# Performance work log

Measured on AMD Instinct MI355X. Metric: run time of the kernel, lower is better.

## Reference

```python
import jax, jax.numpy as jnp
import numpy as np

WS = 8        # window_size
NH = 12       # num_heads


def setup_inputs() -> dict:
    key = jax.random.key(0)
    ks = jax.random.split(key, 9)
    B, C, H, W = 4, 384, 128, 128
    s = 1.0 / np.sqrt(C)
    x = jax.random.normal(ks[0], (B, C, H, W), dtype=jnp.float32)
    Wq = jax.random.normal(ks[1], (C, C), dtype=jnp.float32) * s
    bq = jax.random.normal(ks[2], (C,), dtype=jnp.float32) * 0.01
    Wk = jax.random.normal(ks[3], (C, C), dtype=jnp.float32) * s
    bk = jax.random.normal(ks[4], (C,), dtype=jnp.float32) * 0.01
    Wv = jax.random.normal(ks[5], (C, C), dtype=jnp.float32) * s
    bv = jax.random.normal(ks[6], (C,), dtype=jnp.float32) * 0.01
    Wp = jax.random.normal(ks[7], (C, C), dtype=jnp.float32) * s
    bp = jax.random.normal(ks[8], (C,), dtype=jnp.float32) * 0.01
    return {"x": x, "Wq": Wq, "bq": bq, "Wk": Wk, "bk": bk,
            "Wv": Wv, "bv": bv, "Wp": Wp, "bp": bp}


def reference(x, Wq, bq, Wk, bk, Wv, bv, Wp, bp):
    B, C, H, W = x.shape
    ws2 = WS * WS
    dk = C // NH
    scale = dk ** -0.5

    # window_partition: flat row-major reshape (same semantics as torch's
    # reshape on a contiguous [B,C,H,W] tensor), then permute+view.
    p = x.reshape(B, H // WS, WS, W // WS, WS, C)
    p = jnp.transpose(p, (0, 5, 1, 3, 2, 4))          # [B, C, H/ws, W/ws, ws, ws]
    p = p.reshape(B, C, -1, ws2)                       # [B, C, nW, ws*ws]

    def conv1x1(w, b):  # 1x1 Conv2d on [B,C,nW,ws2]
        return jnp.einsum('bcnw,oc->bonw', p, w) + b[None, :, None, None]

    def heads(t):  # permute(0,2,3,1).contiguous().reshape -> [B, NH, nW, ws2, dk]
        t = jnp.transpose(t, (0, 2, 3, 1))             # [B, nW, ws2, C]
        return t.reshape(B, NH, -1, ws2, dk)           # row-major reinterpretation

    q = heads(conv1x1(Wq, bq))
    k = heads(conv1x1(Wk, bk))
    v = heads(conv1x1(Wv, bv))

    scores = jnp.einsum('bhnqd,bhnkd->bhnqk', q, k) * scale
    attn = jax.nn.softmax(scores, axis=-1)
    o = jnp.einsum('bhnqk,bhnkd->bhnqd', attn, v)      # [B, NH, nW, ws2, dk]
    o = o.reshape(B, -1, ws2, C)                       # [B, nW, ws2, C]

    # window_unpartition
    u = o.reshape(B, -1, WS, WS, C)
    u = jnp.transpose(u, (0, 4, 1, 2, 3))              # [B, C, nW, ws, ws]
    u = u.reshape(B, C, H, W)

    y = jnp.einsum('bchw,oc->bohw', u, Wp) + bp[None, :, None, None]
    return y
```

## Files before the change

kernel.cpp:

```cpp
#include <hip/hip_runtime.h>
#include <hip/hip_bf16.h>
#include <stdint.h>


typedef __bf16 bf16_t;
typedef __bf16 bf16x8 __attribute__((ext_vector_type(8)));
typedef float f32x4 __attribute__((ext_vector_type(4)));

__device__ __forceinline__ void gload_lds16(const void* g, void* l) {
  __builtin_amdgcn_global_load_lds((__attribute__((address_space(1))) void*)(g),
                                   (__attribute__((address_space(3))) void*)(l),
                                   16, 0, 0);
}

__global__ __launch_bounds__(256) void convw_kernel(
    const float* __restrict__ wq, const float* __restrict__ wk,
    const float* __restrict__ wv, const float* __restrict__ wp,
    bf16_t* __restrict__ oq, bf16_t* __restrict__ ok,
    bf16_t* __restrict__ ov, bf16_t* __restrict__ op_) {
  int i = blockIdx.x * 256 + threadIdx.x;
  oq[i] = (bf16_t)wq[i];
  ok[i] = (bf16_t)wk[i];
  ov[i] = (bf16_t)wv[i];
  op_[i] = (bf16_t)wp[i];
}

__device__ __forceinline__ void stageB(const bf16_t* __restrict__ B,
                                       bf16_t* Bs, int k0, int tid) {
  const int lane = tid & 63, wvv = tid >> 6;
  const int s = (lane & 3) ^ ((lane >> 3) & 3);
#pragma unroll
  for (int j = 0; j < 2; ++j) {
    int q = wvv * 128 + j * 64 + lane;
    int row = q >> 2;
    gload_lds16(B + (size_t)row * 384 + k0 + s * 8,
                (char*)Bs + (wvv * 128 + j * 64) * 16);
  }
}

struct ARegs { float4 v0, v1, v2, v3; };

__device__ __forceinline__ ARegs issueA(const float* __restrict__ xr0,
                                        const float* __restrict__ xr1, int k0) {
  ARegs a;
  a.v0 = *(const float4*)(xr0 + k0);
  a.v1 = *(const float4*)(xr0 + k0 + 4);
  a.v2 = *(const float4*)(xr1 + k0);
  a.v3 = *(const float4*)(xr1 + k0 + 4);
  return a;
}

__device__ __forceinline__ void writeA(const ARegs& a, bf16_t* Ab,
                                       int r0loc, int ssw) {
  bf16x8 p0, p1;
  p0[0] = (bf16_t)a.v0.x; p0[1] = (bf16_t)a.v0.y;
  p0[2] = (bf16_t)a.v0.z; p0[3] = (bf16_t)a.v0.w;
  p0[4] = (bf16_t)a.v1.x; p0[5] = (bf16_t)a.v1.y;
  p0[6] = (bf16_t)a.v1.z; p0[7] = (bf16_t)a.v1.w;
  p1[0] = (bf16_t)a.v2.x; p1[1] = (bf16_t)a.v2.y;
  p1[2] = (bf16_t)a.v2.z; p1[3] = (bf16_t)a.v2.w;
  p1[4] = (bf16_t)a.v3.x; p1[5] = (bf16_t)a.v3.y;
  p1[6] = (bf16_t)a.v3.z; p1[7] = (bf16_t)a.v3.w;
  *(bf16x8*)(Ab + r0loc * 32 + ssw * 8) = p0;
  *(bf16x8*)(Ab + (r0loc + 16) * 32 + ssw * 8) = p1;
}

__global__ __launch_bounds__(256) void qkv_gemm(
    const float* __restrict__ x, const bf16_t* __restrict__ Wcat,
    const float* __restrict__ bq, const float* __restrict__ bk,
    const float* __restrict__ bv,
    bf16_t* __restrict__ Qs, bf16_t* __restrict__ Ks, bf16_t* __restrict__ Vs) {
  __shared__ __align__(16) bf16_t L[16384];
  const int tid = threadIdx.x;
  const int F = blockIdx.x;
  const int xcd = F & 7;
  const int t = F >> 3;
  const int j = t % 9;
  const int gq = t / 9;
  const int m0 = (gq * 8 + xcd) * 128;
  const int which = j / 3;
  const int cb = (j % 3) * 128;
  const float* bias = which == 0 ? bq : (which == 1 ? bk : bv);
  bf16_t* Out = which == 0 ? Qs : (which == 1 ? Ks : Vs);
  const bf16_t* Wrows = Wcat + (size_t)j * 128 * 384;

  const int lane = tid & 63, wvv = tid >> 6;
  const int l15 = lane & 15, hi = lane >> 4;
  const int wr = wvv >> 1, wc = wvv & 1;
  const int slot = hi ^ ((l15 >> 1) & 3);
  const int r0loc = wvv * 32 + (lane >> 2);
  const int ssw = (lane & 3) ^ ((lane >> 3) & 3);

  const int b = m0 >> 14;
  const int pp0 = m0 & 16383;
  auto prow = [&](int pp) {
    int n1 = pp >> 10, n3 = (pp >> 6) & 15, w2 = (pp >> 3) & 7, w4 = pp & 7;
    return (size_t)((b << 14) | (n1 << 10) | (w2 << 7) | (n3 << 3) | w4) * 384;
  };
  const float* xr0 = x + prow(pp0 + r0loc) + (lane & 3) * 8;
  const float* xr1 = x + prow(pp0 + r0loc + 16) + (lane & 3) * 8;

  ARegs st0 = issueA(xr0, xr1, 0);
  stageB(Wrows, L + 4096, 0, tid);
  ARegs st1 = issueA(xr0, xr1, 32);
  stageB(Wrows, L + 8192 + 4096, 32, tid);

  f32x4 acc[4][4] = {};
#pragma unroll
  for (int kt = 0; kt < 12; ++kt) {
    bf16_t* Ab = L + (kt & 1) * 8192;
    bf16_t* Bb = Ab + 4096;
    if (kt == 11) asm volatile("s_waitcnt vmcnt(0)" ::: "memory");
    else          asm volatile("s_waitcnt vmcnt(6)" ::: "memory");
    __builtin_amdgcn_sched_barrier(0);
    writeA((kt & 1) ? st1 : st0, Ab, r0loc, ssw);
    asm volatile("s_waitcnt lgkmcnt(0)" ::: "memory");
    __builtin_amdgcn_sched_barrier(0);
    __builtin_amdgcn_s_barrier();
    bf16x8 a[4], bfr[4];
#pragma unroll
    for (int i = 0; i < 4; ++i) {
      a[i] = *(const bf16x8*)(Ab + (wr * 64 + i * 16 + l15) * 32 + slot * 8);
      bfr[i] = *(const bf16x8*)(Bb + (wc * 64 + i * 16 + l15) * 32 + slot * 8);
    }
#pragma unroll
    for (int mi = 0; mi < 4; ++mi)
#pragma unroll
      for (int ni = 0; ni < 4; ++ni)
        acc[mi][ni] = __builtin_amdgcn_mfma_f32_16x16x32_bf16(a[mi], bfr[ni],
                                                              acc[mi][ni], 0, 0, 0);
    asm volatile("s_waitcnt lgkmcnt(0)" ::: "memory");
    __builtin_amdgcn_sched_barrier(0);
    __builtin_amdgcn_s_barrier();
    if (kt + 2 < 12) {
      if (kt & 1) st1 = issueA(xr0, xr1, (kt + 2) * 32);
      else        st0 = issueA(xr0, xr1, (kt + 2) * 32);
      stageB(Wrows, Bb, (kt + 2) * 32, tid);
    }
  }

#pragma unroll
  for (int ni = 0; ni < 4; ++ni) {
    int ch = wc * 64 + ni * 16 + l15;
    float bv_ = bias[cb + ch];
#pragma unroll
    for (int mi = 0; mi < 4; ++mi)
#pragma unroll
      for (int r = 0; r < 4; ++r) {
        int row = wr * 64 + mi * 16 + hi * 4 + r;
        L[row * 128 + ch] = (bf16_t)(acc[mi][ni][r] + bv_);
      }
  }
  __syncthreads();
#pragma unroll
  for (int p = 0; p < 8; ++p) {
    int row = p * 16 + (tid >> 4);
    int ch = (tid & 15) * 8;
    bf16x8 val = *(const bf16x8*)(L + row * 128 + ch);
    *(bf16x8*)(Out + (size_t)(m0 + row) * 384 + cb + ch) = val;
  }
}

__device__ __forceinline__ void stage_tile(const bf16_t* __restrict__ A,
                                           const bf16_t* __restrict__ B,
                                           bf16_t* As, bf16_t* Bs, int k0, int tid) {
  const int lane = tid & 63, wvv = tid >> 6;
  const int s = (lane & 3) ^ ((lane >> 3) & 3);
#pragma unroll
  for (int j = 0; j < 2; ++j) {
    int q = wvv * 128 + j * 64 + lane;
    int row = q >> 2;
    gload_lds16(A + (size_t)row * 384 + k0 + s * 8,
                (char*)As + (wvv * 128 + j * 64) * 16);
    gload_lds16(B + (size_t)row * 384 + k0 + s * 8,
                (char*)Bs + (wvv * 128 + j * 64) * 16);
  }
}

__device__ __forceinline__ void gemm_mainloop(const bf16_t* __restrict__ Arows,
                                              const bf16_t* __restrict__ Brows,
                                              bf16_t* As, bf16_t* Bs,
                                              int tid, f32x4 acc[4][4]) {
  const int lane = tid & 63;
  const int l15 = lane & 15, hi = lane >> 4;
  const int wr = (tid >> 6) >> 1, wc = (tid >> 6) & 1;
  const int slot = hi ^ ((l15 >> 1) & 3);
  stage_tile(Arows, Brows, As, Bs, 0, tid);
  stage_tile(Arows, Brows, As + 4096, Bs + 4096, 32, tid);
#pragma unroll
  for (int kt = 0; kt < 12; ++kt) {
    bf16_t* Ab = As + (kt & 1) * 4096;
    bf16_t* Bb = Bs + (kt & 1) * 4096;
    if (kt == 11) asm volatile("s_waitcnt vmcnt(0)" ::: "memory");
    else          asm volatile("s_waitcnt vmcnt(4)" ::: "memory");
    __builtin_amdgcn_s_barrier();
    bf16x8 a[4], bfr[4];
#pragma unroll
    for (int i = 0; i < 4; ++i) {
      a[i] = *(const bf16x8*)(Ab + (wr * 64 + i * 16 + l15) * 32 + slot * 8);
      bfr[i] = *(const bf16x8*)(Bb + (wc * 64 + i * 16 + l15) * 32 + slot * 8);
    }
#pragma unroll
    for (int mi = 0; mi < 4; ++mi)
#pragma unroll
      for (int ni = 0; ni < 4; ++ni)
        acc[mi][ni] = __builtin_amdgcn_mfma_f32_16x16x32_bf16(a[mi], bfr[ni],
                                                              acc[mi][ni], 0, 0, 0);
    asm volatile("s_waitcnt lgkmcnt(0)" ::: "memory");
    __builtin_amdgcn_sched_barrier(0);
    __builtin_amdgcn_s_barrier();
    if (kt + 2 < 12)
      stage_tile(Arows, Brows, Ab, Bb, (kt + 2) * 32, tid);
  }
}

__global__ __launch_bounds__(64) void attn_kernel(const bf16_t* __restrict__ Q,
                                                  const bf16_t* __restrict__ K,
                                                  const bf16_t* __restrict__ V,
                                                  bf16_t* __restrict__ O) {
  const size_t base = (size_t)blockIdx.x * 2048;
  const bf16_t* q = Q + base;
  const bf16_t* k = K + base;
  const bf16_t* v = V + base;
  bf16_t* o = O + base;
  const int lane = threadIdx.x;
  const int l15 = lane & 15, hi = lane >> 4;

  __shared__ __align__(16) bf16_t Vt[32][72];
  __shared__ __align__(16) bf16_t Ps[64][72];

#pragma unroll
  for (int j = 0; j < 4; ++j) {
    bf16x8 vv = *(const bf16x8*)(v + lane * 32 + j * 8);
#pragma unroll
    for (int e = 0; e < 8; ++e) Vt[j * 8 + e][lane] = vv[e];
  }

  bf16x8 aQ[4], bK[4];
#pragma unroll
  for (int i = 0; i < 4; ++i) {
    aQ[i] = *(const bf16x8*)(q + (i * 16 + l15) * 32 + hi * 8);
    bK[i] = *(const bf16x8*)(k + (i * 16 + l15) * 32 + hi * 8);
  }
  f32x4 sc[4][4] = {};
#pragma unroll
  for (int mi = 0; mi < 4; ++mi)
#pragma unroll
    for (int ni = 0; ni < 4; ++ni)
      sc[mi][ni] = __builtin_amdgcn_mfma_f32_16x16x32_bf16(aQ[mi], bK[ni],
                                                           sc[mi][ni], 0, 0, 0);

  const float SCALE = 0.17677669529663687f;
  float rs[4][4];
#pragma unroll
  for (int mi = 0; mi < 4; ++mi) {
#pragma unroll
    for (int r = 0; r < 4; ++r) {
      float s0 = sc[mi][0][r] * SCALE, s1 = sc[mi][1][r] * SCALE;
      float s2 = sc[mi][2][r] * SCALE, s3 = sc[mi][3][r] * SCALE;
      float mx = fmaxf(fmaxf(s0, s1), fmaxf(s2, s3));
      mx = fmaxf(mx, __shfl_xor(mx, 1));
      mx = fmaxf(mx, __shfl_xor(mx, 2));
      mx = fmaxf(mx, __shfl_xor(mx, 4));
      mx = fmaxf(mx, __shfl_xor(mx, 8));
      float p0 = __expf(s0 - mx), p1 = __expf(s1 - mx);
      float p2 = __expf(s2 - mx), p3 = __expf(s3 - mx);
      int row = mi * 16 + hi * 4 + r;
      Ps[row][0 + l15] = (bf16_t)p0;
      Ps[row][16 + l15] = (bf16_t)p1;
      Ps[row][32 + l15] = (bf16_t)p2;
      Ps[row][48 + l15] = (bf16_t)p3;
      float sum = p0 + p1 + p2 + p3;
      sum += __shfl_xor(sum, 1);
      sum += __shfl_xor(sum, 2);
      sum += __shfl_xor(sum, 4);
      sum += __shfl_xor(sum, 8);
      rs[mi][r] = sum;
    }
  }
  __syncthreads();

  f32x4 oacc[4][2] = {};
#pragma unroll
  for (int mi = 0; mi < 4; ++mi)
#pragma unroll
    for (int ks = 0; ks < 2; ++ks) {
      bf16x8 aP = *(const bf16x8*)(&Ps[mi * 16 + l15][ks * 32 + hi * 8]);
#pragma unroll
      for (int n2 = 0; n2 < 2; ++n2) {
        bf16x8 bV = *(const bf16x8*)(&Vt[n2 * 16 + l15][ks * 32 + hi * 8]);
        oacc[mi][n2] = __builtin_amdgcn_mfma_f32_16x16x32_bf16(aP, bV,
                                                               oacc[mi][n2], 0, 0, 0);
      }
    }
#pragma unroll
  for (int mi = 0; mi < 4; ++mi)
#pragma unroll
    for (int n2 = 0; n2 < 2; ++n2)
#pragma unroll
      for (int r = 0; r < 4; ++r) {
        int row = mi * 16 + hi * 4 + r;
        o[row * 32 + n2 * 16 + l15] = (bf16_t)(oacc[mi][n2][r] / rs[mi][r]);
      }
}

__global__ __launch_bounds__(256) void proj_gemm(const bf16_t* __restrict__ Wpb,
                                                 const bf16_t* __restrict__ O,
                                                 const float* __restrict__ bp,
                                                 float* __restrict__ y) {
  __shared__ __align__(16) bf16_t As[2 * 128 * 32];
  __shared__ __align__(16) bf16_t Bs[2 * 128 * 32];
  const int tid = threadIdx.x;
  const int F = blockIdx.x;
  const int xcd = F & 7;
  const int t = F >> 3;
  const int j = t % 3;
  const int gq = t / 3;
  const int g = gq * 8 + xcd;
  const int n0 = (g & 127) * 128;
  const int b = g >> 7;
  const int m0 = j * 128;
  f32x4 acc[4][4] = {};
  gemm_mainloop(Wpb + (size_t)m0 * 384, O + ((size_t)b * 16384 + n0) * 384,
                As, Bs, tid, acc);
  const int lane = tid & 63, wvv = tid >> 6;
  const int l15 = lane & 15, hi = lane >> 4;
  const int wr = wvv >> 1, wc = wvv & 1;
  float* yb = y + (size_t)b * 6291456;
#pragma unroll
  for (int mi = 0; mi < 4; ++mi)
#pragma unroll
    for (int r = 0; r < 4; ++r) {
      int och = m0 + wr * 64 + mi * 16 + hi * 4 + r;
      float bpv = bp[och];
#pragma unroll
      for (int ni = 0; ni < 4; ++ni) {
        int pix = n0 + wc * 64 + ni * 16 + l15;
        yb[(size_t)och * 16384 + pix] = acc[mi][ni][r] + bpv;
      }
    }
}

extern "C" void kernel_launch(void* const* d_in, const int* in_sizes, int n_in,
                              void* d_out, int out_size, void* d_ws, size_t ws_size,
                              hipStream_t stream) {
  const float* x  = (const float*)d_in[0];
  const float* Wq = (const float*)d_in[1];
  const float* bq = (const float*)d_in[2];
  const float* Wk = (const float*)d_in[3];
  const float* bk = (const float*)d_in[4];
  const float* Wv = (const float*)d_in[5];
  const float* bv = (const float*)d_in[6];
  const float* Wp = (const float*)d_in[7];
  const float* bp = (const float*)d_in[8];
  float* y = (float*)d_out;

  char* ws = (char*)d_ws;
  const size_t SZ = 50331648;
  bf16_t* Ob  = (bf16_t*)(ws);
  bf16_t* Vs  = (bf16_t*)(ws + SZ);
  bf16_t* Wcat = (bf16_t*)(ws + 2 * SZ);
  bf16_t* Wkb = Wcat + 147456;
  bf16_t* Wvb = Wkb + 147456;
  bf16_t* Wpb = Wvb + 147456;
  bf16_t* Qs  = (bf16_t*)d_out;
  bf16_t* Ks  = (bf16_t*)((char*)d_out + SZ);

  convw_kernel<<<576, 256, 0, stream>>>(Wq, Wk, Wv, Wp, Wcat, Wkb, Wvb, Wpb);
  qkv_gemm<<<4608, 256, 0, stream>>>(x, Wcat, bq, bk, bv, Qs, Ks, Vs);
  attn_kernel<<<12288, 64, 0, stream>>>(Qs, Ks, Vs, Ob);
  proj_gemm<<<1536, 256, 0, stream>>>(Wpb, Ob, bp, y);
}
```

Baseline: 203.3 us.

## Fuse QKV GEMM into one persistent-row kernel keeping x tile resident in LDS

The QKV projection now launches one block per 128-row tile of x. Each block converts its full 128x384 activation slab to bf16 once and keeps it in 96KB of dynamic LDS, then sweeps all nine 128-column weight chunks with double-buffered weight staging. This removes the ninefold re-reading and re-conversion of fp32 x across column blocks. The costs are only 512 blocks with low occupancy from the large LDS footprint, and unstaged direct global stores of the output in the epilogue.

```diff
diff --git a/kernel.cpp b/kernel.cpp
--- a/kernel.cpp
+++ b/kernel.cpp
@@ -25,103 +25,100 @@
   op_[i] = (bf16_t)wp[i];
 }
 
-__device__ __forceinline__ void stageB(const bf16_t* __restrict__ B,
-                                       bf16_t* Bs, int k0, int tid) {
-  const int lane = tid & 63, wvv = tid >> 6;
-  const int s = (lane & 3) ^ ((lane >> 3) & 3);
-#pragma unroll
-  for (int j = 0; j < 2; ++j) {
-    int q = wvv * 128 + j * 64 + lane;
-    int row = q >> 2;
-    gload_lds16(B + (size_t)row * 384 + k0 + s * 8,
-                (char*)Bs + (wvv * 128 + j * 64) * 16);
-  }
-}
-
-struct ARegs { float4 v0, v1, v2, v3; };
-
-__device__ __forceinline__ ARegs issueA(const float* __restrict__ xr0,
-                                        const float* __restrict__ xr1, int k0) {
-  ARegs a;
-  a.v0 = *(const float4*)(xr0 + k0);
-  a.v1 = *(const float4*)(xr0 + k0 + 4);
-  a.v2 = *(const float4*)(xr1 + k0);
-  a.v3 = *(const float4*)(xr1 + k0 + 4);
-  return a;
-}
-
-__device__ __forceinline__ void writeA(const ARegs& a, bf16_t* Ab,
-                                       int r0loc, int ssw) {
-  bf16x8 p0, p1;
-  p0[0] = (bf16_t)a.v0.x; p0[1] = (bf16_t)a.v0.y;
-  p0[2] = (bf16_t)a.v0.z; p0[3] = (bf16_t)a.v0.w;
-  p0[4] = (bf16_t)a.v1.x; p0[5] = (bf16_t)a.v1.y;
-  p0[6] = (bf16_t)a.v1.z; p0[7] = (bf16_t)a.v1.w;
-  p1[0] = (bf16_t)a.v2.x; p1[1] = (bf16_t)a.v2.y;
-  p1[2] = (bf16_t)a.v2.z; p1[3] = (bf16_t)a.v2.w;
-  p1[4] = (bf16_t)a.v3.x; p1[5] = (bf16_t)a.v3.y;
-  p1[6] = (bf16_t)a.v3.z; p1[7] = (bf16_t)a.v3.w;
-  *(bf16x8*)(Ab + r0loc * 32 + ssw * 8) = p0;
-  *(bf16x8*)(Ab + (r0loc + 16) * 32 + ssw * 8) = p1;
-}
-
-__global__ __launch_bounds__(256) void qkv_gemm(
+__global__ __launch_bounds__(256) void qkv_fused(
     const float* __restrict__ x, const bf16_t* __restrict__ Wcat,
     const float* __restrict__ bq, const float* __restrict__ bk,
     const float* __restrict__ bv,
     bf16_t* __restrict__ Qs, bf16_t* __restrict__ Ks, bf16_t* __restrict__ Vs) {
-  __shared__ __align__(16) bf16_t L[16384];
+  extern __shared__ __align__(16) char smem[];
+  bf16_t* As = (bf16_t*)smem;
+  bf16_t* Bs = (bf16_t*)(smem + 98304);
+
   const int tid = threadIdx.x;
-  const int F = blockIdx.x;
-  const int xcd = F & 7;
-  const int t = F >> 3;
-  const int j = t % 9;
-  const int gq = t / 9;
-  const int m0 = (gq * 8 + xcd) * 128;
-  const int which = j / 3;
-  const int cb = (j % 3) * 128;
-  const float* bias = which == 0 ? bq : (which == 1 ? bk : bv);
-  bf16_t* Out = which == 0 ? Qs : (which == 1 ? Ks : Vs);
-  const bf16_t* Wrows = Wcat + (size_t)j * 128 * 384;
-
   const int lane = tid & 63, wvv = tid >> 6;
   const int l15 = lane & 15, hi = lane >> 4;
   const int wr = wvv >> 1, wc = wvv & 1;
-  const int slot = hi ^ ((l15 >> 1) & 3);
-  const int r0loc = wvv * 32 + (lane >> 2);
-  const int ssw = (lane & 3) ^ ((lane >> 3) & 3);
-
+  const int slotB = hi ^ ((l15 >> 1) & 3);
+  const int sswB = (lane & 3) ^ ((lane >> 3) & 3);
+
+  const int m0 = blockIdx.x * 128;
   const int b = m0 >> 14;
   const int pp0 = m0 & 16383;
-  auto prow = [&](int pp) {
-    int n1 = pp >> 10, n3 = (pp >> 6) & 15, w2 = (pp >> 3) & 7, w4 = pp & 7;
-    return (size_t)((b << 14) | (n1 << 10) | (w2 << 7) | (n3 << 3) | w4) * 384;
+
+  auto stageB = [&](int s) {
+    int jj = s / 12, kk = s - jj * 12;
+    const bf16_t* src = Wcat + (size_t)jj * 49152 + kk * 32;
+    bf16_t* dst = Bs + (s & 1) * 4096;
+#pragma unroll
+    for (int h = 0; h < 2; ++h) {
+      int qq = wvv * 128 + h * 64 + lane;
+      int row = qq >> 2;
+      gload_lds16(src + (size_t)row * 384 + sswB * 8,
+                  (char*)dst + (wvv * 128 + h * 64) * 16);
+    }
   };
-  const float* xr0 = x + prow(pp0 + r0loc) + (lane & 3) * 8;
-  const float* xr1 = x + prow(pp0 + r0loc + 16) + (lane & 3) * 8;
-
-  ARegs st0 = issueA(xr0, xr1, 0);
-  stageB(Wrows, L + 4096, 0, tid);
-  ARegs st1 = issueA(xr0, xr1, 32);
-  stageB(Wrows, L + 8192 + 4096, 32, tid);
-
+
+  stageB(0);
+  stageB(1);
+
+  {
+    float4 ca[6][2], cb2[6][2];
+    auto issue = [&](float4 (&buf)[6][2], int c) {
+#pragma unroll
+      for (int u = 0; u < 6; ++u) {
+        unsigned gid = (unsigned)(c * 6 + u) * 256u + (unsigned)tid;
+        unsigned r = gid / 48u, g = gid - r * 48u;
+        int pp = pp0 + (int)r;
+        int n1 = pp >> 10, n3 = (pp >> 6) & 15, w2 = (pp >> 3) & 7, w4 = pp & 7;
+        const float* src = x +
+            (size_t)((b << 14) | (n1 << 10) | (w2 << 7) | (n3 << 3) | w4) * 384 +
+            g * 8;
+        buf[u][0] = *(const float4*)(src);
+        buf[u][1] = *(const float4*)(src + 4);
+      }
+    };
+    auto consume = [&](float4 (&buf)[6][2], int c) {
+#pragma unroll
+      for (int u = 0; u < 6; ++u) {
+        unsigned gid = (unsigned)(c * 6 + u) * 256u + (unsigned)tid;
+        unsigned r = gid / 48u, g = gid - r * 48u;
+        bf16x8 p;
+        p[0] = (bf16_t)buf[u][0].x; p[1] = (bf16_t)buf[u][0].y;
+        p[2] = (bf16_t)buf[u][0].z; p[3] = (bf16_t)buf[u][0].w;
+        p[4] = (bf16_t)buf[u][1].x; p[5] = (bf16_t)buf[u][1].y;
+        p[6] = (bf16_t)buf[u][1].z; p[7] = (bf16_t)buf[u][1].w;
+        *(bf16x8*)(As + r * 384 + (g ^ (r & 7u)) * 8) = p;
+      }
+    };
+    issue(ca, 0);
+    issue(cb2, 1);
+    consume(ca, 0);
+    issue(ca, 2);
+    consume(cb2, 1);
+    issue(cb2, 3);
+    consume(ca, 2);
+    consume(cb2, 3);
+  }
+  __syncthreads();
+
+  const f32x4 fz = {0.f, 0.f, 0.f, 0.f};
   f32x4 acc[4][4] = {};
-#pragma unroll
-  for (int kt = 0; kt < 12; ++kt) {
-    bf16_t* Ab = L + (kt & 1) * 8192;
-    bf16_t* Bb = Ab + 4096;
-    if (kt == 11) asm volatile("s_waitcnt vmcnt(0)" ::: "memory");
-    else          asm volatile("s_waitcnt vmcnt(6)" ::: "memory");
-    __builtin_amdgcn_sched_barrier(0);
-    writeA((kt & 1) ? st1 : st0, Ab, r0loc, ssw);
-    asm volatile("s_waitcnt lgkmcnt(0)" ::: "memory");
-    __builtin_amdgcn_sched_barrier(0);
+
+  for (int s = 0; s < 108; ++s) {
+    const int j = s / 12;
+    const int kt = s - j * 12;
+    if (s == 107) asm volatile("s_waitcnt vmcnt(0)" ::: "memory");
+    else          asm volatile("s_waitcnt vmcnt(2)" ::: "memory");
     __builtin_amdgcn_s_barrier();
+
+    const bf16_t* Bb = Bs + (s & 1) * 4096;
     bf16x8 a[4], bfr[4];
 #pragma unroll
     for (int i = 0; i < 4; ++i) {
-      a[i] = *(const bf16x8*)(Ab + (wr * 64 + i * 16 + l15) * 32 + slot * 8);
-      bfr[i] = *(const bf16x8*)(Bb + (wc * 64 + i * 16 + l15) * 32 + slot * 8);
+      int r = wr * 64 + i * 16 + l15;
+      int gr = (4 * kt + hi) ^ (l15 & 7);
+      a[i] = *(const bf16x8*)(As + r * 384 + gr * 8);
+      bfr[i] = *(const bf16x8*)(Bb + (wc * 64 + i * 16 + l15) * 32 + slotB * 8);
     }
 #pragma unroll
     for (int mi = 0; mi < 4; ++mi)
@@ -132,32 +129,29 @@
     asm volatile("s_waitcnt lgkmcnt(0)" ::: "memory");
     __builtin_amdgcn_sched_barrier(0);
     __builtin_amdgcn_s_barrier();
-    if (kt + 2 < 12) {
-      if (kt & 1) st1 = issueA(xr0, xr1, (kt + 2) * 32);
-      else        st0 = issueA(xr0, xr1, (kt + 2) * 32);
-      stageB(Wrows, Bb, (kt + 2) * 32, tid);
-    }
-  }
-
-#pragma unroll
-  for (int ni = 0; ni < 4; ++ni) {
-    int ch = wc * 64 + ni * 16 + l15;
-    float bv_ = bias[cb + ch];
-#pragma unroll
-    for (int mi = 0; mi < 4; ++mi)
-#pragma unroll
-      for (int r = 0; r < 4; ++r) {
-        int row = wr * 64 + mi * 16 + hi * 4 + r;
-        L[row * 128 + ch] = (bf16_t)(acc[mi][ni][r] + bv_);
-      }
-  }
-  __syncthreads();
-#pragma unroll
-  for (int p = 0; p < 8; ++p) {
-    int row = p * 16 + (tid >> 4);
-    int ch = (tid & 15) * 8;
-    bf16x8 val = *(const bf16x8*)(L + row * 128 + ch);
-    *(bf16x8*)(Out + (size_t)(m0 + row) * 384 + cb + ch) = val;
+    if (s + 2 < 108) stageB(s + 2);
+
+    if (kt == 11) {
+      const float* bias = (j < 3) ? bq : (j < 6) ? bk : bv;
+      bf16_t* Out = (j < 3) ? Qs : (j < 6) ? Ks : Vs;
+      const int cb = (j % 3) * 128;
+#pragma unroll
+      for (int ni = 0; ni < 4; ++ni) {
+        int ch = wc * 64 + ni * 16 + l15;
+        float bv_ = bias[cb + ch];
+#pragma unroll
+        for (int mi = 0; mi < 4; ++mi)
+#pragma unroll
+          for (int rr = 0; rr < 4; ++rr) {
+            int row = m0 + wr * 64 + mi * 16 + hi * 4 + rr;
+            Out[(size_t)row * 384 + cb + ch] = (bf16_t)(acc[mi][ni][rr] + bv_);
+          }
+      }
+#pragma unroll
+      for (int mi = 0; mi < 4; ++mi)
+#pragma unroll
+        for (int ni = 0; ni < 4; ++ni) acc[mi][ni] = fz;
+    }
   }
 }
 
@@ -366,8 +360,11 @@
   bf16_t* Qs  = (bf16_t*)d_out;
   bf16_t* Ks  = (bf16_t*)((char*)d_out + SZ);
 
+  hipFuncSetAttribute((const void*)qkv_fused,
+                      hipFuncAttributeMaxDynamicSharedMemorySize, 114688);
+
   convw_kernel<<<576, 256, 0, stream>>>(Wq, Wk, Wv, Wp, Wcat, Wkb, Wvb, Wpb);
-  qkv_gemm<<<4608, 256, 0, stream>>>(x, Wcat, bq, bk, bv, Qs, Ks, Vs);
+  qkv_fused<<<512, 256, 114688, stream>>>(x, Wcat, bq, bk, bv, Qs, Ks, Vs);
   attn_kernel<<<12288, 64, 0, stream>>>(Qs, Ks, Vs, Ob);
   proj_gemm<<<1536, 256, 0, stream>>>(Wpb, Ob, bp, y);
 }
```

Result: slower. 210.4 us (+3.4%).
